# Kernel tuning notes

Hardware: AMD Instinct MI355X
Metric: run time of the kernel (lower is better)

## Reference

```python
import jax, jax.numpy as jnp
import numpy as np

EPS = 1e-3

def _block_orthogonal(num_rows, num_cols, seed=0):
    # Faithful to orthogonal_matrix(): stack of QR-orthogonalized square blocks.
    rng = np.random.default_rng(seed)
    blocks = []
    n_full = num_rows // num_cols
    for _ in range(n_full):
        q, _ = np.linalg.qr(rng.standard_normal((num_cols, num_cols)).astype(np.float32))
        blocks.append(q.T)
    remain = num_rows - n_full * num_cols
    if remain > 0:
        q, _ = np.linalg.qr(rng.standard_normal((num_cols, num_cols)).astype(np.float32))
        blocks.append(q.T[:remain])
    return jnp.asarray(np.concatenate(blocks, axis=0), dtype=jnp.float32)


def setup_inputs() -> dict:
    key = jax.random.key(0)
    k1, k2, k3 = jax.random.split(key, 3)
    B, H, L, D = 4, 16, 4096, 64
    num_rows = int(D * np.log(D))  # 266
    return {
        "q": jax.random.normal(k1, (B, H, L, D), dtype=jnp.float32),
        "k": jax.random.normal(k2, (B, H, L, D), dtype=jnp.float32),
        "v": jax.random.normal(k3, (B, H, L, D), dtype=jnp.float32),
        "proj_mat": _block_orthogonal(num_rows, D),  # [266, 64]
    }


def _feature_map(x, proj_t):
    # x: [b,h,l,d], proj_t: [d,m] -> [b,h,l,m]; kernel = relu, +epsilon
    return jax.nn.relu(jnp.einsum('bhld,dm->bhlm', x, proj_t)) + EPS


def reference(q, k, v, proj_mat):
    proj_t = proj_mat.T                     # [d, m]
    qp = _feature_map(q, proj_t)            # [b,h,l,m]
    kp = _feature_map(k, proj_t)            # [b,h,l,m]
    k_sum = jnp.sum(kp, axis=-2)            # [b,h,m]
    d_inv = 1.0 / jnp.einsum('bhlm,bhm->bhl', qp, k_sum)   # [b,h,l]
    kv = jnp.einsum('bhlm,bhld->bhmd', kp, v)              # [b,h,m,d]
    qkv = jnp.einsum('bhlm,bhmd->bhld', qp, kv)            # [b,h,l,d]
    return qkv * d_inv[..., None]
```

## Files before the change

kernel.cpp:

```cpp
#include <hip/hip_runtime.h>

typedef __bf16 bf16;
typedef bf16 bf16x2 __attribute__((ext_vector_type(2)));
typedef bf16 bf16x4 __attribute__((ext_vector_type(4)));
typedef bf16 bf16x8 __attribute__((ext_vector_type(8)));
typedef float f32x4 __attribute__((ext_vector_type(4)));
typedef float f32x16 __attribute__((ext_vector_type(16)));
typedef unsigned int u32;
typedef u32 u32x4 __attribute__((ext_vector_type(4)));
typedef float4 f4;

constexpr int BHN = 64;
constexpr int LN  = 4096;
constexpr int DN  = 64;
constexpr int MN  = 266;
constexpr int MP  = 320;
constexpr int STR = 72;
constexpr int KVS = 328;
constexpr int TL  = 128;
constexpr int NLQ = 4;
constexpr int NTQ = LN / (NLQ * TL);
#define EPSF 1e-3f

#define MFMA32(A, B, C) __builtin_amdgcn_mfma_f32_32x32x16_bf16(A, B, C, 0, 0, 0)

__device__ __forceinline__ u32 cvt_pk_bf16(float lo, float hi) {
  u32 r;
  asm("v_cvt_pk_bf16_f32 %0, %1, %2" : "=v"(r) : "v"(lo), "v"(hi));
  return r;
}

#define T12_TRANSFORM(f, kb0, kb1)                                   \
  {                                                                  \
    u32 w0 = cvt_pk_bf16(f[0], f[1]);                                \
    u32 w1 = cvt_pk_bf16(f[2], f[3]);                                \
    u32 w2 = cvt_pk_bf16(f[4], f[5]);                                \
    u32 w3 = cvt_pk_bf16(f[6], f[7]);                                \
    u32 w4 = cvt_pk_bf16(f[8], f[9]);                                \
    u32 w5 = cvt_pk_bf16(f[10], f[11]);                              \
    u32 w6 = cvt_pk_bf16(f[12], f[13]);                              \
    u32 w7 = cvt_pk_bf16(f[14], f[15]);                              \
    asm("v_permlane32_swap_b32 %0, %1" : "+v"(w0), "+v"(w2));        \
    asm("v_permlane32_swap_b32 %0, %1" : "+v"(w1), "+v"(w3));        \
    asm("v_permlane32_swap_b32 %0, %1" : "+v"(w4), "+v"(w6));        \
    asm("v_permlane32_swap_b32 %0, %1" : "+v"(w5), "+v"(w7));        \
    u32x4 a0_ = {w0, w1, w2, w3};                                    \
    u32x4 a1_ = {w4, w5, w6, w7};                                    \
    kb0 = __builtin_bit_cast(bf16x8, a0_);                           \
    kb1 = __builtin_bit_cast(bf16x8, a1_);                           \
  }

__global__ __launch_bounds__(640, 2) void perf_kv_fused(
    const float* __restrict__ kg, const float* __restrict__ vg,
    const float* __restrict__ proj, float* __restrict__ kv_part,
    float* __restrict__ ksum_part)
{
  __shared__ __align__(16) bf16 k_lds[TL * STR];
  __shared__ __align__(16) bf16 vt_lds[64 * 128];

  const int t    = threadIdx.x;
  const int wid  = t >> 6;
  const int lane = t & 63;
  const int ln31 = lane & 31;
  const int hi   = lane >> 5;
  const int mc   = wid % 5;
  const int h    = wid / 5;
  const int lq   = blockIdx.x & 3;
  const int bh   = blockIdx.x >> 2;
  const int m0   = mc * 64;

  bf16x8 pb[4];
  {
    const int m = m0 + h * 32 + ln31;
#pragma unroll
    for (int ks = 0; ks < 4; ++ks) {
      bf16x8 w = {};
      if (m < MN) {
        const float* p = proj + m * 64 + ks * 16 + hi * 8;
        f4 a = *(const f4*)p;
        f4 b = *(const f4*)(p + 4);
        w = (bf16x8){(bf16)a.x, (bf16)a.y, (bf16)a.z, (bf16)a.w,
                     (bf16)b.x, (bf16)b.y, (bf16)b.z, (bf16)b.w};
      }
      pb[ks] = w;
    }
  }

  f32x16 acc0 = (f32x16){};
  f32x16 acc1 = (f32x16){};
  float ksum_acc = 0.f;

  const f4* kg4 = (const f4*)kg + ((size_t)bh * LN) * 16;
  const f4* vg4 = (const f4*)vg + ((size_t)bh * LN) * 16;

  f4 kreg[4], vra[2], vrb[2];

  auto LOAD = [&](int tile) {
    const int l0 = (lq * NTQ + tile) * TL;
    if (t < 512) {
#pragma unroll
      for (int i2 = 0; i2 < 4; ++i2) {
        int idx = t + i2 * 512;
        kreg[i2] = kg4[(l0 + (idx >> 4)) * 16 + (idx & 15)];
      }
#pragma unroll
      for (int i2 = 0; i2 < 2; ++i2) {
        int u = t + i2 * 512;
        int lb2 = u >> 4, d4 = u & 15;
        vra[i2] = vg4[(l0 + lb2 * 2) * 16 + d4];
        vrb[i2] = vg4[(l0 + lb2 * 2 + 1) * 16 + d4];
      }
    }
  };
  auto VTW = [&](int r, int c) -> bf16* {
    return &vt_lds[r * 128 + (c ^ ((r & 15) << 3))];
  };
  auto WRITE = [&]() {
    if (t < 512) {
#pragma unroll
      for (int i2 = 0; i2 < 4; ++i2) {
        int idx = t + i2 * 512;
        int row = idx >> 4, d4 = idx & 15;
        f4 val = kreg[i2];
        bf16x4 w = {(bf16)val.x, (bf16)val.y, (bf16)val.z, (bf16)val.w};
        *(bf16x4*)&k_lds[row * STR + d4 * 4] = w;
      }
#pragma unroll
      for (int i2 = 0; i2 < 2; ++i2) {
        int u = t + i2 * 512;
        int lb2 = u >> 4, d4 = u & 15;
        f4 a = vra[i2], b2 = vrb[i2];
        bf16x2 w0 = {(bf16)a.x, (bf16)b2.x};
        bf16x2 w1 = {(bf16)a.y, (bf16)b2.y};
        bf16x2 w2 = {(bf16)a.z, (bf16)b2.z};
        bf16x2 w3 = {(bf16)a.w, (bf16)b2.w};
        *(bf16x2*)VTW(d4 * 4 + 0, lb2 * 2) = w0;
        *(bf16x2*)VTW(d4 * 4 + 1, lb2 * 2) = w1;
        *(bf16x2*)VTW(d4 * 4 + 2, lb2 * 2) = w2;
        *(bf16x2*)VTW(d4 * 4 + 3, lb2 * 2) = w3;
      }
    }
  };

  LOAD(0);
  for (int tile = 0; tile < NTQ; ++tile) {
    __syncthreads();
    WRITE();
    if (tile < NTQ - 1) LOAD(tile + 1);
    __syncthreads();

#pragma unroll
    for (int s4 = 0; s4 < 4; ++s4) {
      bf16x8 ka[4];
#pragma unroll
      for (int ks = 0; ks < 4; ++ks)
        ka[ks] = *(const bf16x8*)&k_lds[(s4 * 32 + ln31) * STR + ks * 16 + hi * 8];
      bf16x8 va00 = *(const bf16x8*)VTW(ln31, s4 * 32 + hi * 8);
      bf16x8 va01 = *(const bf16x8*)VTW(ln31, s4 * 32 + 16 + hi * 8);
      bf16x8 va10 = *(const bf16x8*)VTW(32 + ln31, s4 * 32 + hi * 8);
      bf16x8 va11 = *(const bf16x8*)VTW(32 + ln31, s4 * 32 + 16 + hi * 8);

      f32x16 f = (f32x16){};
#pragma unroll
      for (int ks = 0; ks < 4; ++ks) f = MFMA32(ka[ks], pb[ks], f);
#pragma unroll
      for (int i2 = 0; i2 < 16; ++i2) f[i2] = fmaxf(f[i2], 0.f) + EPSF;
      ksum_acc += f[0] + f[1] + f[2] + f[3] + f[4] + f[5] + f[6] + f[7]
                + f[8] + f[9] + f[10] + f[11] + f[12] + f[13] + f[14] + f[15];

      bf16x8 kb0, kb1;
      T12_TRANSFORM(f, kb0, kb1)
      acc0 = MFMA32(va00, kb0, acc0);
      acc0 = MFMA32(va01, kb1, acc0);
      acc1 = MFMA32(va10, kb0, acc1);
      acc1 = MFMA32(va11, kb1, acc1);
    }
  }

  {
    const int m = m0 + h * 32 + ln31;
    float* base = kv_part + ((size_t)lq * BHN + bh) * 64 * MP;
#pragma unroll
    for (int r = 0; r < 16; ++r) {
      const int d0 = (r & 3) + 8 * (r >> 2) + 4 * hi;
      base[(size_t)d0 * MP + m] = acc0[r];
      base[(size_t)(32 + d0) * MP + m] = acc1[r];
    }
    float rr = ksum_acc + __shfl_xor(ksum_acc, 32);
    if (hi == 0) ksum_part[((size_t)lq * BHN + bh) * MP + m] = rr;
  }
}

__global__ __launch_bounds__(256) void perf_reduce(
    const float* __restrict__ kv_part, const float* __restrict__ ksum_part,
    bf16* __restrict__ kv_b, float* __restrict__ ksum_ws)
{
  constexpr int KV4 = BHN * DN * MP / 4;
  constexpr int KS  = BHN * MP;
  constexpr size_t PS  = (size_t)BHN * DN * MP;
  constexpr size_t PSK = (size_t)BHN * MP;

  int idx = blockIdx.x * 256 + threadIdx.x;
  if (idx < KV4) {
    const f4* p = (const f4*)kv_part;
    f4 v0 = p[idx];
    f4 v1 = p[idx + PS / 4];
    f4 v2 = p[idx + 2 * (PS / 4)];
    f4 v3 = p[idx + 3 * (PS / 4)];
    f4 sv = {v0.x + v1.x + v2.x + v3.x, v0.y + v1.y + v2.y + v3.y,
             v0.z + v1.z + v2.z + v3.z, v0.w + v1.w + v2.w + v3.w};
    int m = (idx * 4) % MP;
    bf16x4 w;
    w[0] = (m + 0 < MN) ? (bf16)sv.x : (bf16)0.f;
    w[1] = (m + 1 < MN) ? (bf16)sv.y : (bf16)0.f;
    w[2] = (m + 2 < MN) ? (bf16)sv.z : (bf16)0.f;
    w[3] = (m + 3 < MN) ? (bf16)sv.w : (bf16)0.f;
    *(bf16x4*)&kv_b[idx * 4] = w;
  } else if (idx < KV4 + KS) {
    int p = idx - KV4;
    int m = p % MP;
    float v = ksum_part[p] + ksum_part[p + PSK] + ksum_part[p + 2 * PSK]
            + ksum_part[p + 3 * PSK];
    ksum_ws[p] = (m < MN) ? v : 0.f;
  }
}

__global__ __launch_bounds__(512, 2) void perf_out_mfma32(
    const float* __restrict__ qg, const float* __restrict__ proj,
    const bf16* __restrict__ kvb, const float* __restrict__ ksum_ws,
    float* __restrict__ outg)
{
  __shared__ __align__(16) bf16 pj_lds[MP * STR];
  __shared__ __align__(16) bf16 kv_lds[DN * KVS];
  __shared__ __align__(16) float ksum_lds[MP];
  __shared__ float dp_lds[8 * 64];

  const int t    = threadIdx.x;
  const int wid  = t >> 6;
  const int lane = t & 63;
  const int ln31 = lane & 31;
  const int hi   = lane >> 5;
  const int bh   = blockIdx.y;
  const int lbase = blockIdx.x * 1024;

  {
    const f4* projv = (const f4*)proj;
#pragma unroll
    for (int i = 0; i < 10; ++i) {
      int idx = t + i * 512;
      int r = idx >> 4, c4 = idx & 15;
      f4 v = {0.f, 0.f, 0.f, 0.f};
      if (r < MN) v = projv[r * 16 + c4];
      bf16x4 w = {(bf16)v.x, (bf16)v.y, (bf16)v.z, (bf16)v.w};
      *(bf16x4*)&pj_lds[r * STR + c4 * 4] = w;
    }
  }
  for (int idx = t; idx < DN * 40; idx += 512) {
    int r = idx / 40, cc = idx % 40;
    *(bf16x8*)&kv_lds[r * KVS + cc * 8] =
        *(const bf16x8*)&kvb[((size_t)bh * DN + r) * MP + cc * 8];
  }
  if (t < MP) ksum_lds[t] = ksum_ws[bh * MP + t];
  __syncthreads();

  for (int rnd = 0; rnd < 2; ++rnd) {
    const int lw = lbase + rnd * 512 + wid * 64;

    bf16x8 qb[2][4];
#pragma unroll
    for (int lt = 0; lt < 2; ++lt)
#pragma unroll
      for (int ks = 0; ks < 4; ++ks) {
        const float* qp_ = qg + ((size_t)bh * LN + lw + lt * 32 + ln31) * 64 + ks * 16 + hi * 8;
        f4 a = *(const f4*)qp_;
        f4 b = *(const f4*)(qp_ + 4);
        qb[lt][ks] = (bf16x8){(bf16)a.x, (bf16)a.y, (bf16)a.z, (bf16)a.w,
                              (bf16)b.x, (bf16)b.y, (bf16)b.z, (bf16)b.w};
      }

    f32x16 oc[2][2];
    oc[0][0] = (f32x16){}; oc[0][1] = (f32x16){};
    oc[1][0] = (f32x16){}; oc[1][1] = (f32x16){};
    float dp[2] = {0.f, 0.f};

    for (int mc = 0; mc < 5; ++mc) {
      f32x16 c2[2][2];
      c2[0][0] = (f32x16){}; c2[0][1] = (f32x16){};
      c2[1][0] = (f32x16){}; c2[1][1] = (f32x16){};
#pragma unroll
      for (int ks = 0; ks < 4; ++ks) {
        bf16x8 pa0 = *(const bf16x8*)&pj_lds[(mc * 64 + ln31) * STR + ks * 16 + hi * 8];
        bf16x8 pa1 = *(const bf16x8*)&pj_lds[(mc * 64 + 32 + ln31) * STR + ks * 16 + hi * 8];
        c2[0][0] = MFMA32(pa0, qb[0][ks], c2[0][0]);
        c2[1][0] = MFMA32(pa0, qb[1][ks], c2[1][0]);
        c2[0][1] = MFMA32(pa1, qb[0][ks], c2[0][1]);
        c2[1][1] = MFMA32(pa1, qb[1][ks], c2[1][1]);
      }
#pragma unroll
      for (int mt = 0; mt < 2; ++mt) {
        const int mb = mc * 64 + mt * 32 + 4 * hi;
        f32x4 kq0 = *(const f32x4*)&ksum_lds[mb + 0];
        f32x4 kq1 = *(const f32x4*)&ksum_lds[mb + 8];
        f32x4 kq2 = *(const f32x4*)&ksum_lds[mb + 16];
        f32x4 kq3 = *(const f32x4*)&ksum_lds[mb + 24];
        bf16x8 A[2][2];
#pragma unroll
        for (int lt = 0; lt < 2; ++lt) {
          f32x16 f = c2[lt][mt];
#pragma unroll
          for (int i = 0; i < 16; ++i) f[i] = fmaxf(f[i], 0.f) + EPSF;
          dp[lt] += f[0] * kq0[0] + f[1] * kq0[1] + f[2] * kq0[2] + f[3] * kq0[3]
                  + f[4] * kq1[0] + f[5] * kq1[1] + f[6] * kq1[2] + f[7] * kq1[3]
                  + f[8] * kq2[0] + f[9] * kq2[1] + f[10] * kq2[2] + f[11] * kq2[3]
                  + f[12] * kq3[0] + f[13] * kq3[1] + f[14] * kq3[2] + f[15] * kq3[3];
          bf16x8 kb0, kb1;
          T12_TRANSFORM(f, kb0, kb1)
          A[lt][0] = kb0;
          A[lt][1] = kb1;
        }
#pragma unroll
        for (int kk = 0; kk < 2; ++kk) {
          const int mo = mc * 64 + (mt * 2 + kk) * 16 + hi * 8;
          bf16x8 kb0 = *(const bf16x8*)&kv_lds[ln31 * KVS + mo];
          bf16x8 kb1 = *(const bf16x8*)&kv_lds[(32 + ln31) * KVS + mo];
          oc[0][0] = MFMA32(A[0][kk], kb0, oc[0][0]);
          oc[1][0] = MFMA32(A[1][kk], kb0, oc[1][0]);
          oc[0][1] = MFMA32(A[0][kk], kb1, oc[0][1]);
          oc[1][1] = MFMA32(A[1][kk], kb1, oc[1][1]);
        }
      }
    }

#pragma unroll
    for (int lt = 0; lt < 2; ++lt) {
      float r = dp[lt];
      r += __shfl_xor(r, 32);
      dp_lds[wid * 64 + lt * 32 + ln31] = r;
    }
#pragma unroll
    for (int lt = 0; lt < 2; ++lt) {
#pragma unroll
      for (int rg = 0; rg < 4; ++rg) {
        f32x4 dv = *(const f32x4*)&dp_lds[wid * 64 + lt * 32 + 8 * rg + 4 * hi];
        f32x4 di = {1.f / dv[0], 1.f / dv[1], 1.f / dv[2], 1.f / dv[3]};
#pragma unroll
        for (int dt = 0; dt < 2; ++dt) {
#pragma unroll
          for (int j = 0; j < 4; ++j) {
            int l = lw + lt * 32 + 8 * rg + 4 * hi + j;
            outg[((size_t)bh * LN + l) * DN + dt * 32 + ln31] = oc[lt][dt][4 * rg + j] * di[j];
          }
        }
      }
    }
  }
}

extern "C" void kernel_launch(void* const* d_in, const int* in_sizes, int n_in,
                              void* d_out, int out_size, void* d_ws, size_t ws_size,
                              hipStream_t stream)
{
  const float* q    = (const float*)d_in[0];
  const float* k    = (const float*)d_in[1];
  const float* v    = (const float*)d_in[2];
  const float* proj = (const float*)d_in[3];
  float* out = (float*)d_out;

  float* kv_part   = (float*)d_ws;
  float* ksum_part = kv_part + (size_t)NLQ * BHN * DN * MP;
  float* ksum_ws   = ksum_part + (size_t)NLQ * BHN * MP;
  bf16*  kv_b      = (bf16*)(ksum_ws + (size_t)BHN * MP);

  perf_kv_fused<<<NLQ * BHN, 640, 0, stream>>>(k, v, proj, kv_part, ksum_part);

  constexpr int RED_ITEMS = BHN * DN * MP / 4 + BHN * MP;
  perf_reduce<<<(RED_ITEMS + 255) / 256, 256, 0, stream>>>(kv_part, ksum_part, kv_b, ksum_ws);

  perf_out_mfma32<<<dim3(LN / 1024, BHN), 512, 0, stream>>>(q, proj, kv_b, ksum_ws, out);
}
```

Before: 92.89 us.

## Fuse partial KV reduction into output kernel and remap blocks across XCDs

Drops the separate reduce kernel. Each output block now sums the four fp32 L-partitions of kv and ksum for its head while loading them into LDS, and converts to bf16 there. The grid becomes 1-D, with block ids remapped so the four blocks of one head land on the same XCD and can share L2 for the partial reads. This saves a launch and a workspace round trip, but each head's partials are now read four times instead of once.

```diff
diff --git a/kernel.cpp b/kernel.cpp
--- a/kernel.cpp
+++ b/kernel.cpp
@@ -191,43 +191,9 @@
   }
 }
 
-__global__ __launch_bounds__(256) void perf_reduce(
-    const float* __restrict__ kv_part, const float* __restrict__ ksum_part,
-    bf16* __restrict__ kv_b, float* __restrict__ ksum_ws)
-{
-  constexpr int KV4 = BHN * DN * MP / 4;
-  constexpr int KS  = BHN * MP;
-  constexpr size_t PS  = (size_t)BHN * DN * MP;
-  constexpr size_t PSK = (size_t)BHN * MP;
-
-  int idx = blockIdx.x * 256 + threadIdx.x;
-  if (idx < KV4) {
-    const f4* p = (const f4*)kv_part;
-    f4 v0 = p[idx];
-    f4 v1 = p[idx + PS / 4];
-    f4 v2 = p[idx + 2 * (PS / 4)];
-    f4 v3 = p[idx + 3 * (PS / 4)];
-    f4 sv = {v0.x + v1.x + v2.x + v3.x, v0.y + v1.y + v2.y + v3.y,
-             v0.z + v1.z + v2.z + v3.z, v0.w + v1.w + v2.w + v3.w};
-    int m = (idx * 4) % MP;
-    bf16x4 w;
-    w[0] = (m + 0 < MN) ? (bf16)sv.x : (bf16)0.f;
-    w[1] = (m + 1 < MN) ? (bf16)sv.y : (bf16)0.f;
-    w[2] = (m + 2 < MN) ? (bf16)sv.z : (bf16)0.f;
-    w[3] = (m + 3 < MN) ? (bf16)sv.w : (bf16)0.f;
-    *(bf16x4*)&kv_b[idx * 4] = w;
-  } else if (idx < KV4 + KS) {
-    int p = idx - KV4;
-    int m = p % MP;
-    float v = ksum_part[p] + ksum_part[p + PSK] + ksum_part[p + 2 * PSK]
-            + ksum_part[p + 3 * PSK];
-    ksum_ws[p] = (m < MN) ? v : 0.f;
-  }
-}
-
 __global__ __launch_bounds__(512, 2) void perf_out_mfma32(
     const float* __restrict__ qg, const float* __restrict__ proj,
-    const bf16* __restrict__ kvb, const float* __restrict__ ksum_ws,
+    const float* __restrict__ kv_part, const float* __restrict__ ksum_part,
     float* __restrict__ outg)
 {
   __shared__ __align__(16) bf16 pj_lds[MP * STR];
@@ -240,8 +206,12 @@
   const int lane = t & 63;
   const int ln31 = lane & 31;
   const int hi   = lane >> 5;
-  const int bh   = blockIdx.y;
-  const int lbase = blockIdx.x * 1024;
+
+  const int id   = blockIdx.x;
+  const int xcd  = id & 7, slot = id >> 3;
+  const int bh   = xcd + (slot >> 2) * 8;
+  const int lb   = slot & 3;
+  const int lbase = lb * 1024;
 
   {
     const f4* projv = (const f4*)proj;
@@ -255,12 +225,36 @@
       *(bf16x4*)&pj_lds[r * STR + c4 * 4] = w;
     }
   }
-  for (int idx = t; idx < DN * 40; idx += 512) {
-    int r = idx / 40, cc = idx % 40;
-    *(bf16x8*)&kv_lds[r * KVS + cc * 8] =
-        *(const bf16x8*)&kvb[((size_t)bh * DN + r) * MP + cc * 8];
-  }
-  if (t < MP) ksum_lds[t] = ksum_ws[bh * MP + t];
+  {
+    constexpr size_t LQS = (size_t)BHN * DN * MP;
+    const float* base = kv_part + (size_t)bh * DN * MP;
+#pragma unroll
+    for (int i = 0; i < 5; ++i) {
+      int idx = t + i * 512;
+      int r = idx / 40, cc = idx % 40;
+      const float* p = base + (size_t)r * MP + cc * 8;
+      f4 a0 = *(const f4*)(p);            f4 b0 = *(const f4*)(p + 4);
+      f4 a1 = *(const f4*)(p + LQS);      f4 b1 = *(const f4*)(p + LQS + 4);
+      f4 a2 = *(const f4*)(p + 2 * LQS);  f4 b2 = *(const f4*)(p + 2 * LQS + 4);
+      f4 a3 = *(const f4*)(p + 3 * LQS);  f4 b3 = *(const f4*)(p + 3 * LQS + 4);
+      float s[8] = {a0.x + a1.x + a2.x + a3.x, a0.y + a1.y + a2.y + a3.y,
+                    a0.z + a1.z + a2.z + a3.z, a0.w + a1.w + a2.w + a3.w,
+                    b0.x + b1.x + b2.x + b3.x, b0.y + b1.y + b2.y + b3.y,
+                    b0.z + b1.z + b2.z + b3.z, b0.w + b1.w + b2.w + b3.w};
+      const int mbase = cc * 8;
+      bf16x8 w;
+#pragma unroll
+      for (int j = 0; j < 8; ++j)
+        w[j] = (mbase + j < MN) ? (bf16)s[j] : (bf16)0.f;
+      *(bf16x8*)&kv_lds[r * KVS + cc * 8] = w;
+    }
+  }
+  if (t < MP) {
+    constexpr size_t LQK = (size_t)BHN * MP;
+    const float* p = ksum_part + (size_t)bh * MP + t;
+    float v = p[0] + p[LQK] + p[2 * LQK] + p[3 * LQK];
+    ksum_lds[t] = (t < MN) ? v : 0.f;
+  }
   __syncthreads();
 
   for (int rnd = 0; rnd < 2; ++rnd) {
@@ -368,13 +362,7 @@
 
   float* kv_part   = (float*)d_ws;
   float* ksum_part = kv_part + (size_t)NLQ * BHN * DN * MP;
-  float* ksum_ws   = ksum_part + (size_t)NLQ * BHN * MP;
-  bf16*  kv_b      = (bf16*)(ksum_ws + (size_t)BHN * MP);
 
   perf_kv_fused<<<NLQ * BHN, 640, 0, stream>>>(k, v, proj, kv_part, ksum_part);
-
-  constexpr int RED_ITEMS = BHN * DN * MP / 4 + BHN * MP;
-  perf_reduce<<<(RED_ITEMS + 255) / 256, 256, 0, stream>>>(kv_part, ksum_part, kv_b, ksum_ws);
-
-  perf_out_mfma32<<<dim3(LN / 1024, BHN), 512, 0, stream>>>(q, proj, kv_b, ksum_ws, out);
+  perf_out_mfma32<<<256, 512, 0, stream>>>(q, proj, kv_part, ksum_part, out);
 }
```

Measured after the change: 89.59 us (median of 2 runs). 1.04x faster.
